# Optimization experiments

Measured on AMD Instinct MI355X. Metric: run time of the kernel, lower is better.

## Reference

```python
import jax, jax.numpy as jnp
import numpy as np

B, S, D = 2, 2048, 1024
H = 16
HD = D // H
MLP = 4096
EPS_LN = 1e-6
EPS_NORM = 1e-12
LOG_MAX = float(np.log(1.0 / 0.01))  # clamp cap for logit_scale


def setup_inputs() -> dict:
    key = jax.random.key(0)
    ks = jax.random.split(key, 12)
    sd = 0.02
    return {
        "x": jax.random.normal(ks[0], (B, S, D), jnp.float32),
        "wq": jax.random.normal(ks[1], (D, D), jnp.float32) * sd,
        "bq": jnp.zeros((D,), jnp.float32),
        "wk": jax.random.normal(ks[2], (D, D), jnp.float32) * sd,
        "bk": jnp.zeros((D,), jnp.float32),
        "wv": jax.random.normal(ks[3], (D, D), jnp.float32) * sd,
        "bv": jnp.zeros((D,), jnp.float32),
        "wo": jax.random.normal(ks[4], (D, D), jnp.float32) * sd,
        "bo": jnp.zeros((D,), jnp.float32),
        "w1": jax.random.normal(ks[5], (D, MLP), jnp.float32) * sd,
        "b1": jax.random.normal(ks[6], (MLP,), jnp.float32) * 1e-6,
        "w2": jax.random.normal(ks[7], (MLP, D), jnp.float32) * sd,
        "b2": jax.random.normal(ks[8], (D,), jnp.float32) * 1e-6,
        "ln1_g": jnp.ones((D,), jnp.float32),
        "ln1_b": jnp.zeros((D,), jnp.float32),
        "ln2_g": jnp.ones((D,), jnp.float32),
        "ln2_b": jnp.zeros((D,), jnp.float32),
        "logit_scale": jnp.log(10.0 * jnp.ones((H, 1, 1), jnp.float32)),
    }


def _layernorm(x, g, b):
    mu = jnp.mean(x, axis=-1, keepdims=True)
    var = jnp.var(x, axis=-1, keepdims=True)
    return (x - mu) * jax.lax.rsqrt(var + EPS_LN) * g + b


def _l2norm(x):
    n = jnp.linalg.norm(x, axis=-1, keepdims=True)
    return x / jnp.maximum(n, EPS_NORM)


def _split_heads(t):  # [B,S,D] -> [B,H,S,HD]
    return t.reshape(B, S, H, HD).transpose(0, 2, 1, 3)


def reference(x, wq, bq, wk, bk, wv, bv, wo, bo, w1, b1, w2, b2,
              ln1_g, ln1_b, ln2_g, ln2_b, logit_scale):
    h = x
    xn = _layernorm(x, ln1_g, ln1_b)
    q = _split_heads(xn @ wq + bq)
    k = _split_heads(xn @ wk + bk)
    v = _split_heads(xn @ wv + bv)
    # cosine attention: L2-normalize q,k, scale by clamped learnable exp temp
    scores = jnp.einsum("bhqd,bhkd->bhqk", _l2norm(q), _l2norm(k))
    scale = jnp.exp(jnp.minimum(logit_scale, LOG_MAX))  # [H,1,1]
    scores = scores * scale
    probs = jax.nn.softmax(scores, axis=-1)
    ctx = jnp.einsum("bhqk,bhkd->bhqd", probs, v)
    ctx = ctx.transpose(0, 2, 1, 3).reshape(B, S, D)
    x = ctx @ wo + bo + h
    h = x
    xn = _layernorm(x, ln2_g, ln2_b)
    y = jax.nn.gelu(xn @ w1 + b1, approximate=False) @ w2 + b2
    return y + h
```

## Files before the change

### kernel.cpp

```cpp
#include <hip/hip_runtime.h>
#include <hip/hip_bf16.h>
#include <math.h>

typedef unsigned short u16;
typedef unsigned int u32;
typedef __attribute__((ext_vector_type(8))) short bf16x8;
typedef __attribute__((ext_vector_type(4))) float f32x4;

#define S_LEN 2048
#define DM 1024
#define NH 16
#define HD 64
#define MLPD 4096
#define BSZ 2
#define NROWS (BSZ * S_LEN)
#define LOGMAX 4.60517018598809f

__device__ __forceinline__ u16 f2bf(float f) {
  u32 u = __float_as_uint(f);
  u32 r = (u + 0x7fffu + ((u >> 16) & 1u)) >> 16;
  return (u16)r;
}
__device__ __forceinline__ float bf2f(u16 h) { return __uint_as_float(((u32)h) << 16); }
__device__ __forceinline__ u32 pk2(float a, float b) {
  return (u32)f2bf(a) | ((u32)f2bf(b) << 16);
}
__device__ __forceinline__ void gld16(const void* g, void* l) {
  __builtin_amdgcn_global_load_lds(
      (const __attribute__((address_space(1))) void*)g,
      (__attribute__((address_space(3))) void*)l, 16, 0, 0);
}

__global__ __launch_bounds__(256) void ln_bf16(const float* __restrict__ x,
                                               const float* __restrict__ g,
                                               const float* __restrict__ b,
                                               u16* __restrict__ out) {
  const int row = blockIdx.x;
  const int t = threadIdx.x;
  const float* xr = x + (size_t)row * DM;
  float4 v = *reinterpret_cast<const float4*>(xr + t * 4);
  float s = v.x + v.y + v.z + v.w;
  float s2 = v.x * v.x + v.y * v.y + v.z * v.z + v.w * v.w;
#pragma unroll
  for (int off = 32; off > 0; off >>= 1) {
    s += __shfl_down(s, off);
    s2 += __shfl_down(s2, off);
  }
  __shared__ float red[8];
  __shared__ float mv[2];
  const int wid = t >> 6, lane = t & 63;
  if (lane == 0) { red[wid] = s; red[wid + 4] = s2; }
  __syncthreads();
  if (t == 0) {
    float ts = red[0] + red[1] + red[2] + red[3];
    float ts2 = red[4] + red[5] + red[6] + red[7];
    float mu = ts * (1.0f / DM);
    float var = ts2 * (1.0f / DM) - mu * mu;
    mv[0] = mu;
    mv[1] = rsqrtf(var + 1e-6f);
  }
  __syncthreads();
  const float mu = mv[0], rs = mv[1];
  float4 gv = *reinterpret_cast<const float4*>(g + t * 4);
  float4 bv = *reinterpret_cast<const float4*>(b + t * 4);
  float o0 = (v.x - mu) * rs * gv.x + bv.x;
  float o1 = (v.y - mu) * rs * gv.y + bv.y;
  float o2 = (v.z - mu) * rs * gv.z + bv.z;
  float o3 = (v.w - mu) * rs * gv.w + bv.w;
  uint2 o;
  o.x = pk2(o0, o1);
  o.y = pk2(o2, o3);
  *reinterpret_cast<uint2*>(out + (size_t)row * DM + t * 4) = o;
}

__global__ __launch_bounds__(256) void prep_weights(
    const float* __restrict__ wq, const float* __restrict__ wk, const float* __restrict__ wv,
    const float* __restrict__ wo, const float* __restrict__ w1, const float* __restrict__ w2,
    const float* __restrict__ bq, const float* __restrict__ bk, const float* __restrict__ bv,
    u16* __restrict__ wqkv_t, u16* __restrict__ wo_t, u16* __restrict__ w1_t,
    u16* __restrict__ w2_t, float* __restrict__ bqkv) {
  const int tid = threadIdx.x;
  int bid = blockIdx.x;
  if (bid < 12) {
    int i = bid * 256 + tid;
    bqkv[i] = i < 1024 ? bq[i] : (i < 2048 ? bk[i - 1024] : bv[i - 2048]);
  }
  const float* src;
  u16* dst;
  int K, N;
  if (bid < 768) {
    int m = bid >> 8;
    src = (m == 0) ? wq : (m == 1 ? wk : wv);
    dst = wqkv_t + (size_t)m * 1024 * 1024;
    K = 1024; N = 1024;
    bid &= 255;
  } else if (bid < 1024) {
    src = wo; dst = wo_t; K = 1024; N = 1024; bid -= 768;
  } else if (bid < 2048) {
    src = w1; dst = w1_t; K = 1024; N = 4096; bid -= 1024;
  } else {
    src = w2; dst = w2_t; K = 4096; N = 1024; bid -= 2048;
  }
  const int ktiles = K >> 6;
  const int k0 = (bid % ktiles) << 6, n0 = (bid / ktiles) << 6;
  __shared__ float tile[64][65];
#pragma unroll
  for (int p = 0; p < 4; ++p) {
    int r = p * 16 + (tid >> 4), c = (tid & 15) * 4;
    *reinterpret_cast<float4*>(&tile[r][c]) =
        *reinterpret_cast<const float4*>(&src[(size_t)(k0 + r) * N + n0 + c]);
  }
  __syncthreads();
#pragma unroll
  for (int p = 0; p < 4; ++p) {
    int n = p * 16 + (tid >> 4), k = (tid & 15) * 4;
    uint2 o;
    o.x = pk2(tile[k][n], tile[k + 1][n]);
    o.y = pk2(tile[k + 2][n], tile[k + 3][n]);
    *reinterpret_cast<uint2*>(&dst[(size_t)(n0 + n) * K + k0 + k]) = o;
  }
}

#define EPI_BIAS 0
#define EPI_GELU 1
#define EPI_RES 2

template <int EPI, int OUTBF>
__global__ __launch_bounds__(256) void gemm_bf16(
    const u16* __restrict__ A, const u16* __restrict__ Bt,
    const float* __restrict__ bias, const float* __restrict__ res,
    void* __restrict__ Cout, int M, int N, int K) {
  __shared__ u16 As[128 * 32];
  __shared__ u16 Bs[128 * 32];
  const int tid = threadIdx.x;
  const int wid = tid >> 6, lane = tid & 63;
  const int n0 = blockIdx.x * 128, m0 = blockIdx.y * 128;
  const int wr = wid >> 1, wc = wid & 1;

  f32x4 acc[4][4];
#pragma unroll
  for (int mi = 0; mi < 4; ++mi)
#pragma unroll
    for (int ni = 0; ni < 4; ++ni)
#pragma unroll
      for (int r = 0; r < 4; ++r) acc[mi][ni][r] = 0.0f;

  const int srow = lane >> 2;
  const int skc = (lane & 3) * 8;

  for (int k0 = 0; k0 < K; k0 += 32) {
#pragma unroll
    for (int i = 0; i < 2; ++i) {
      int c = wid * 2 + i;
      gld16(&A[(size_t)(m0 + c * 16 + srow) * K + k0 + skc], &As[c * 512]);
      gld16(&Bt[(size_t)(n0 + c * 16 + srow) * K + k0 + skc], &Bs[c * 512]);
    }
    __syncthreads();
    const int fr = lane & 15, fg = (lane >> 4) * 8;
    bf16x8 af[4], bfr[4];
#pragma unroll
    for (int mi = 0; mi < 4; ++mi)
      af[mi] = *reinterpret_cast<const bf16x8*>(&As[(wr * 64 + mi * 16 + fr) * 32 + fg]);
#pragma unroll
    for (int ni = 0; ni < 4; ++ni)
      bfr[ni] = *reinterpret_cast<const bf16x8*>(&Bs[(wc * 64 + ni * 16 + fr) * 32 + fg]);
#pragma unroll
    for (int mi = 0; mi < 4; ++mi)
#pragma unroll
      for (int ni = 0; ni < 4; ++ni)
        acc[mi][ni] =
            __builtin_amdgcn_mfma_f32_16x16x32_bf16(af[mi], bfr[ni], acc[mi][ni], 0, 0, 0);
    __syncthreads();
  }

  const int col0 = n0 + wc * 64 + (lane & 15);
  const int r4 = (lane >> 4) * 4;
#pragma unroll
  for (int ni = 0; ni < 4; ++ni) {
    const int col = col0 + ni * 16;
    const float bb = bias[col];
#pragma unroll
    for (int mi = 0; mi < 4; ++mi) {
      const int row = m0 + wr * 64 + mi * 16 + r4;
#pragma unroll
      for (int r = 0; r < 4; ++r) {
        float v = acc[mi][ni][r] + bb;
        if (EPI == EPI_GELU) v = 0.5f * v * (1.0f + erff(v * 0.70710678118654752f));
        if (EPI == EPI_RES) v += res[(size_t)(row + r) * N + col];
        if (OUTBF)
          ((u16*)Cout)[(size_t)(row + r) * N + col] = f2bf(v);
        else
          ((float*)Cout)[(size_t)(row + r) * N + col] = v;
      }
    }
  }
}

__global__ __launch_bounds__(256) void flash_mfma(const u16* __restrict__ qkv,
                                                  const float* __restrict__ lsc,
                                                  u16* __restrict__ ctx) {
  __shared__ u16 Ks[64 * 72];
  __shared__ u16 Vt[64 * 72];
  __shared__ u16 Ps[128 * 72];
  const int tid = threadIdx.x;
  const int wq = tid >> 6, lane = tid & 63;
  const int q0 = blockIdx.x * 128;
  const int bh = blockIdx.y, b = bh >> 4, h = bh & 15;
  const float scale = __expf(fminf(lsc[h], LOGMAX));
  const int fr = lane & 15, fgq = lane >> 4;

  bf16x8 qf[2][2];
#pragma unroll
  for (int qs = 0; qs < 2; ++qs) {
    float qv[2][8];
    float ssq = 0.0f;
#pragma unroll
    for (int ds = 0; ds < 2; ++ds) {
      const u16* src = qkv + (size_t)(b * S_LEN + q0 + wq * 32 + qs * 16 + fr) * 3072 +
                       h * 64 + ds * 32 + fgq * 8;
      uint4 u = *reinterpret_cast<const uint4*>(src);
      qv[ds][0] = bf2f(u.x & 0xffff); qv[ds][1] = bf2f(u.x >> 16);
      qv[ds][2] = bf2f(u.y & 0xffff); qv[ds][3] = bf2f(u.y >> 16);
      qv[ds][4] = bf2f(u.z & 0xffff); qv[ds][5] = bf2f(u.z >> 16);
      qv[ds][6] = bf2f(u.w & 0xffff); qv[ds][7] = bf2f(u.w >> 16);
#pragma unroll
      for (int j = 0; j < 8; ++j) ssq += qv[ds][j] * qv[ds][j];
    }
    ssq += __shfl_xor(ssq, 16);
    ssq += __shfl_xor(ssq, 32);
    float inv = 1.0f / fmaxf(sqrtf(ssq), 1e-12f);
#pragma unroll
    for (int ds = 0; ds < 2; ++ds)
#pragma unroll
      for (int j = 0; j < 8; ++j) qf[qs][ds][j] = (short)f2bf(qv[ds][j] * inv);
  }

  float den[2][4];
  f32x4 octx[2][4];
#pragma unroll
  for (int qs = 0; qs < 2; ++qs)
#pragma unroll
    for (int r = 0; r < 4; ++r) {
      den[qs][r] = 0.0f;
      octx[qs][r][0] = octx[qs][r][1] = octx[qs][r][2] = octx[qs][r][3] = 0.0f;
    }

  const int sr = tid >> 2, sseg = tid & 3;

  for (int kt = 0; kt < S_LEN / 64; ++kt) {
    {
      const u16* gk = qkv + (size_t)(b * S_LEN + kt * 64 + sr) * 3072 + 1024 + h * 64 + sseg * 8;
      uint4 u0 = *reinterpret_cast<const uint4*>(gk);
      uint4 u1 = *reinterpret_cast<const uint4*>(gk + 32);
      float kv[16];
      kv[0] = bf2f(u0.x & 0xffff); kv[1] = bf2f(u0.x >> 16);
      kv[2] = bf2f(u0.y & 0xffff); kv[3] = bf2f(u0.y >> 16);
      kv[4] = bf2f(u0.z & 0xffff); kv[5] = bf2f(u0.z >> 16);
      kv[6] = bf2f(u0.w & 0xffff); kv[7] = bf2f(u0.w >> 16);
      kv[8]  = bf2f(u1.x & 0xffff); kv[9]  = bf2f(u1.x >> 16);
      kv[10] = bf2f(u1.y & 0xffff); kv[11] = bf2f(u1.y >> 16);
      kv[12] = bf2f(u1.z & 0xffff); kv[13] = bf2f(u1.z >> 16);
      kv[14] = bf2f(u1.w & 0xffff); kv[15] = bf2f(u1.w >> 16);
      float ssk = 0.0f;
#pragma unroll
      for (int j = 0; j < 16; ++j) ssk += kv[j] * kv[j];
      ssk += __shfl_xor(ssk, 1);
      ssk += __shfl_xor(ssk, 2);
      float inv = 1.0f / fmaxf(sqrtf(ssk), 1e-12f);
      uint4 o;
      o.x = pk2(kv[0] * inv, kv[1] * inv);
      o.y = pk2(kv[2] * inv, kv[3] * inv);
      o.z = pk2(kv[4] * inv, kv[5] * inv);
      o.w = pk2(kv[6] * inv, kv[7] * inv);
      *reinterpret_cast<uint4*>(&Ks[sr * 72 + sseg * 8]) = o;
      o.x = pk2(kv[8] * inv, kv[9] * inv);
      o.y = pk2(kv[10] * inv, kv[11] * inv);
      o.z = pk2(kv[12] * inv, kv[13] * inv);
      o.w = pk2(kv[14] * inv, kv[15] * inv);
      *reinterpret_cast<uint4*>(&Ks[sr * 72 + 32 + sseg * 8]) = o;
      uint4 vv0 = *reinterpret_cast<const uint4*>(gk + 1024);
      uint4 vv1 = *reinterpret_cast<const uint4*>(gk + 1024 + 32);
      u16 ve[16] = {(u16)(vv0.x & 0xffff), (u16)(vv0.x >> 16), (u16)(vv0.y & 0xffff),
                    (u16)(vv0.y >> 16),    (u16)(vv0.z & 0xffff), (u16)(vv0.z >> 16),
                    (u16)(vv0.w & 0xffff), (u16)(vv0.w >> 16),
                    (u16)(vv1.x & 0xffff), (u16)(vv1.x >> 16), (u16)(vv1.y & 0xffff),
                    (u16)(vv1.y >> 16),    (u16)(vv1.z & 0xffff), (u16)(vv1.z >> 16),
                    (u16)(vv1.w & 0xffff), (u16)(vv1.w >> 16)};
#pragma unroll
      for (int j = 0; j < 8; ++j) {
        Vt[(sseg * 8 + j) * 72 + sr] = ve[j];
        Vt[(32 + sseg * 8 + j) * 72 + sr] = ve[8 + j];
      }
    }
    __syncthreads();

    f32x4 sc[2][4];
#pragma unroll
    for (int qs = 0; qs < 2; ++qs)
#pragma unroll
      for (int ks = 0; ks < 4; ++ks)
        sc[qs][ks][0] = sc[qs][ks][1] = sc[qs][ks][2] = sc[qs][ks][3] = 0.0f;
#pragma unroll
    for (int ks = 0; ks < 4; ++ks)
#pragma unroll
      for (int ds = 0; ds < 2; ++ds) {
        bf16x8 kf = *reinterpret_cast<const bf16x8*>(&Ks[(ks * 16 + fr) * 72 + ds * 32 + fgq * 8]);
#pragma unroll
        for (int qs = 0; qs < 2; ++qs)
          sc[qs][ks] = __builtin_amdgcn_mfma_f32_16x16x32_bf16(qf[qs][ds], kf, sc[qs][ks], 0, 0, 0);
      }

#pragma unroll
    for (int qs = 0; qs < 2; ++qs)
#pragma unroll
      for (int r = 0; r < 4; ++r) {
        const int prow = wq * 32 + qs * 16 + fgq * 4 + r;
        float ps = 0.0f;
#pragma unroll
        for (int ks = 0; ks < 4; ++ks) {
          float p = __expf(scale * (sc[qs][ks][r] - 1.0f));
          Ps[prow * 72 + ks * 16 + fr] = f2bf(p);
          ps += p;
        }
        ps += __shfl_xor(ps, 1);
        ps += __shfl_xor(ps, 2);
        ps += __shfl_xor(ps, 4);
        ps += __shfl_xor(ps, 8);
        den[qs][r] += ps;
      }

#pragma unroll
    for (int kvs = 0; kvs < 2; ++kvs) {
      bf16x8 pf0 = *reinterpret_cast<const bf16x8*>(&Ps[(wq * 32 + fr) * 72 + kvs * 32 + fgq * 8]);
      bf16x8 pf1 =
          *reinterpret_cast<const bf16x8*>(&Ps[(wq * 32 + 16 + fr) * 72 + kvs * 32 + fgq * 8]);
#pragma unroll
      for (int dsb = 0; dsb < 4; ++dsb) {
        bf16x8 vf = *reinterpret_cast<const bf16x8*>(&Vt[(dsb * 16 + fr) * 72 + kvs * 32 + fgq * 8]);
        octx[0][dsb] = __builtin_amdgcn_mfma_f32_16x16x32_bf16(pf0, vf, octx[0][dsb], 0, 0, 0);
        octx[1][dsb] = __builtin_amdgcn_mfma_f32_16x16x32_bf16(pf1, vf, octx[1][dsb], 0, 0, 0);
      }
    }
    __syncthreads();
  }

#pragma unroll
  for (int qs = 0; qs < 2; ++qs)
#pragma unroll
    for (int r = 0; r < 4; ++r) {
      float inv = 1.0f / den[qs][r];
      const int row = q0 + wq * 32 + qs * 16 + fgq * 4 + r;
#pragma unroll
      for (int dsb = 0; dsb < 4; ++dsb)
        ctx[(size_t)(b * S_LEN + row) * DM + h * 64 + dsb * 16 + fr] =
            f2bf(octx[qs][dsb][r] * inv);
    }
}

extern "C" void kernel_launch(void* const* d_in, const int* in_sizes, int n_in,
                              void* d_out, int out_size, void* d_ws, size_t ws_size,
                              hipStream_t stream) {
  const float* x    = (const float*)d_in[0];
  const float* wq   = (const float*)d_in[1];
  const float* bq   = (const float*)d_in[2];
  const float* wk   = (const float*)d_in[3];
  const float* bk   = (const float*)d_in[4];
  const float* wv   = (const float*)d_in[5];
  const float* bv   = (const float*)d_in[6];
  const float* wo   = (const float*)d_in[7];
  const float* bo   = (const float*)d_in[8];
  const float* w1   = (const float*)d_in[9];
  const float* b1   = (const float*)d_in[10];
  const float* w2   = (const float*)d_in[11];
  const float* b2   = (const float*)d_in[12];
  const float* ln1g = (const float*)d_in[13];
  const float* ln1b = (const float*)d_in[14];
  const float* ln2g = (const float*)d_in[15];
  const float* ln2b = (const float*)d_in[16];
  const float* lsc  = (const float*)d_in[17];

  char* ws = (char*)d_ws;
  u16* wqkv_t = (u16*)(ws + 0);
  u16* wo_t   = (u16*)(ws + 6291456);
  u16* w1_t   = (u16*)(ws + 8388608);
  u16* w2_t   = (u16*)(ws + 16777216);
  float* bqkv = (float*)(ws + 25165824);
  u16* xn     = (u16*)(ws + 25178112);
  u16* ctx    = (u16*)(ws + 33566720);
  float* x2   = (float*)(ws + 41955328);
  u16* qkv    = (u16*)(ws + 58732544);
  u16* h1     = qkv;

  prep_weights<<<dim3(3072), dim3(256), 0, stream>>>(wq, wk, wv, wo, w1, w2, bq, bk, bv,
                                                     wqkv_t, wo_t, w1_t, w2_t, bqkv);
  ln_bf16<<<dim3(NROWS), dim3(256), 0, stream>>>(x, ln1g, ln1b, xn);
  gemm_bf16<EPI_BIAS, 1><<<dim3(3072 / 128, NROWS / 128), dim3(256), 0, stream>>>(
      xn, wqkv_t, bqkv, nullptr, qkv, NROWS, 3072, 1024);
  flash_mfma<<<dim3(S_LEN / 128, BSZ * NH), dim3(256), 0, stream>>>(qkv, lsc, ctx);
  gemm_bf16<EPI_RES, 0><<<dim3(1024 / 128, NROWS / 128), dim3(256), 0, stream>>>(
      ctx, wo_t, bo, x, x2, NROWS, 1024, 1024);
  ln_bf16<<<dim3(NROWS), dim3(256), 0, stream>>>(x2, ln2g, ln2b, xn);
  gemm_bf16<EPI_GELU, 1><<<dim3(4096 / 128, NROWS / 128), dim3(256), 0, stream>>>(
      xn, w1_t, b1, nullptr, h1, NROWS, 4096, 1024);
  gemm_bf16<EPI_RES, 0><<<dim3(1024 / 128, NROWS / 128), dim3(256), 0, stream>>>(
      h1, w2_t, b2, x2, (float*)d_out, NROWS, 1024, 4096);
}
```

Measured before the change: 488.1 us.

## Fuse Q/K L2-normalization and V transpose into QKV GEMM epilogue

```diff
diff --git a/kernel.cpp b/kernel.cpp
--- a/kernel.cpp
+++ b/kernel.cpp
@@ -124,12 +124,14 @@
 #define EPI_BIAS 0
 #define EPI_GELU 1
 #define EPI_RES 2
+#define EPI_QKV 3
 
 template <int EPI, int OUTBF>
 __global__ __launch_bounds__(256) void gemm_bf16(
     const u16* __restrict__ A, const u16* __restrict__ Bt,
     const float* __restrict__ bias, const float* __restrict__ res,
-    void* __restrict__ Cout, int M, int N, int K) {
+    void* __restrict__ Cout, u16* __restrict__ qkx, u16* __restrict__ vtx,
+    int M, int N, int K) {
   __shared__ u16 As[128 * 32];
   __shared__ u16 Bs[128 * 32];
   const int tid = threadIdx.x;
@@ -175,10 +177,51 @@
 
   const int col0 = n0 + wc * 64 + (lane & 15);
   const int r4 = (lane >> 4) * 4;
+
+  if constexpr (EPI == EPI_QKV) {
+    float bias4[4];
+#pragma unroll
+    for (int ni = 0; ni < 4; ++ni) bias4[ni] = bias[col0 + ni * 16];
+    const bool isV = (n0 + wc * 64) >= 2048;
+#pragma unroll
+    for (int mi = 0; mi < 4; ++mi) {
+#pragma unroll
+      for (int r = 0; r < 4; ++r) {
+        const int row = m0 + wr * 64 + mi * 16 + r4 + r;
+        float v[4];
+#pragma unroll
+        for (int ni = 0; ni < 4; ++ni) v[ni] = acc[mi][ni][r] + bias4[ni];
+        if (!isV) {
+          float ss = v[0] * v[0] + v[1] * v[1] + v[2] * v[2] + v[3] * v[3];
+          ss += __shfl_xor(ss, 1);
+          ss += __shfl_xor(ss, 2);
+          ss += __shfl_xor(ss, 4);
+          ss += __shfl_xor(ss, 8);
+          float inv = 1.0f / fmaxf(sqrtf(ss), 1e-12f);
+#pragma unroll
+          for (int ni = 0; ni < 4; ++ni)
+            qkx[(size_t)row * 2048 + col0 + ni * 16] = f2bf(v[ni] * inv);
+        } else {
+          const int b = row >> 11, sl = row & 2047;
+#pragma unroll
+          for (int ni = 0; ni < 4; ++ni) {
+            const int col = col0 + ni * 16;
+            const int h = (col - 2048) >> 6, d = col & 63;
+            vtx[((size_t)(b * NH + h) * HD + d) * S_LEN + sl] = f2bf(v[ni]);
+          }
+        }
+      }
+    }
+    return;
+  }
+
+  float bias8[4];
+#pragma unroll
+  for (int ni = 0; ni < 4; ++ni) bias8[ni] = bias[col0 + ni * 16];
 #pragma unroll
   for (int ni = 0; ni < 4; ++ni) {
     const int col = col0 + ni * 16;
-    const float bb = bias[col];
+    const float bb = bias8[ni];
 #pragma unroll
     for (int mi = 0; mi < 4; ++mi) {
       const int row = m0 + wr * 64 + mi * 16 + r4;
@@ -196,7 +239,8 @@
   }
 }
 
-__global__ __launch_bounds__(256) void flash_mfma(const u16* __restrict__ qkv,
+__global__ __launch_bounds__(256) void flash_mfma(const u16* __restrict__ qk,
+                                                  const u16* __restrict__ vt,
                                                   const float* __restrict__ lsc,
                                                   u16* __restrict__ ctx) {
   __shared__ u16 Ks[64 * 72];
@@ -211,29 +255,12 @@
 
   bf16x8 qf[2][2];
 #pragma unroll
-  for (int qs = 0; qs < 2; ++qs) {
-    float qv[2][8];
-    float ssq = 0.0f;
-#pragma unroll
-    for (int ds = 0; ds < 2; ++ds) {
-      const u16* src = qkv + (size_t)(b * S_LEN + q0 + wq * 32 + qs * 16 + fr) * 3072 +
-                       h * 64 + ds * 32 + fgq * 8;
-      uint4 u = *reinterpret_cast<const uint4*>(src);
-      qv[ds][0] = bf2f(u.x & 0xffff); qv[ds][1] = bf2f(u.x >> 16);
-      qv[ds][2] = bf2f(u.y & 0xffff); qv[ds][3] = bf2f(u.y >> 16);
-      qv[ds][4] = bf2f(u.z & 0xffff); qv[ds][5] = bf2f(u.z >> 16);
-      qv[ds][6] = bf2f(u.w & 0xffff); qv[ds][7] = bf2f(u.w >> 16);
-#pragma unroll
-      for (int j = 0; j < 8; ++j) ssq += qv[ds][j] * qv[ds][j];
-    }
-    ssq += __shfl_xor(ssq, 16);
-    ssq += __shfl_xor(ssq, 32);
-    float inv = 1.0f / fmaxf(sqrtf(ssq), 1e-12f);
+  for (int qs = 0; qs < 2; ++qs)
 #pragma unroll
     for (int ds = 0; ds < 2; ++ds)
-#pragma unroll
-      for (int j = 0; j < 8; ++j) qf[qs][ds][j] = (short)f2bf(qv[ds][j] * inv);
-  }
+      qf[qs][ds] = *reinterpret_cast<const bf16x8*>(
+          &qk[(size_t)(b * S_LEN + q0 + wq * 32 + qs * 16 + fr) * 2048 + h * HD + ds * 32 +
+              fgq * 8]);
 
   float den[2][4];
   f32x4 octx[2][4];
@@ -249,48 +276,16 @@
 
   for (int kt = 0; kt < S_LEN / 64; ++kt) {
     {
-      const u16* gk = qkv + (size_t)(b * S_LEN + kt * 64 + sr) * 3072 + 1024 + h * 64 + sseg * 8;
-      uint4 u0 = *reinterpret_cast<const uint4*>(gk);
-      uint4 u1 = *reinterpret_cast<const uint4*>(gk + 32);
-      float kv[16];
-      kv[0] = bf2f(u0.x & 0xffff); kv[1] = bf2f(u0.x >> 16);
-      kv[2] = bf2f(u0.y & 0xffff); kv[3] = bf2f(u0.y >> 16);
-      kv[4] = bf2f(u0.z & 0xffff); kv[5] = bf2f(u0.z >> 16);
-      kv[6] = bf2f(u0.w & 0xffff); kv[7] = bf2f(u0.w >> 16);
-      kv[8]  = bf2f(u1.x & 0xffff); kv[9]  = bf2f(u1.x >> 16);
-      kv[10] = bf2f(u1.y & 0xffff); kv[11] = bf2f(u1.y >> 16);
-      kv[12] = bf2f(u1.z & 0xffff); kv[13] = bf2f(u1.z >> 16);
-      kv[14] = bf2f(u1.w & 0xffff); kv[15] = bf2f(u1.w >> 16);
-      float ssk = 0.0f;
-#pragma unroll
-      for (int j = 0; j < 16; ++j) ssk += kv[j] * kv[j];
-      ssk += __shfl_xor(ssk, 1);
-      ssk += __shfl_xor(ssk, 2);
-      float inv = 1.0f / fmaxf(sqrtf(ssk), 1e-12f);
-      uint4 o;
-      o.x = pk2(kv[0] * inv, kv[1] * inv);
-      o.y = pk2(kv[2] * inv, kv[3] * inv);
-      o.z = pk2(kv[4] * inv, kv[5] * inv);
-      o.w = pk2(kv[6] * inv, kv[7] * inv);
-      *reinterpret_cast<uint4*>(&Ks[sr * 72 + sseg * 8]) = o;
-      o.x = pk2(kv[8] * inv, kv[9] * inv);
-      o.y = pk2(kv[10] * inv, kv[11] * inv);
-      o.z = pk2(kv[12] * inv, kv[13] * inv);
-      o.w = pk2(kv[14] * inv, kv[15] * inv);
-      *reinterpret_cast<uint4*>(&Ks[sr * 72 + 32 + sseg * 8]) = o;
-      uint4 vv0 = *reinterpret_cast<const uint4*>(gk + 1024);
-      uint4 vv1 = *reinterpret_cast<const uint4*>(gk + 1024 + 32);
-      u16 ve[16] = {(u16)(vv0.x & 0xffff), (u16)(vv0.x >> 16), (u16)(vv0.y & 0xffff),
-                    (u16)(vv0.y >> 16),    (u16)(vv0.z & 0xffff), (u16)(vv0.z >> 16),
-                    (u16)(vv0.w & 0xffff), (u16)(vv0.w >> 16),
-                    (u16)(vv1.x & 0xffff), (u16)(vv1.x >> 16), (u16)(vv1.y & 0xffff),
-                    (u16)(vv1.y >> 16),    (u16)(vv1.z & 0xffff), (u16)(vv1.z >> 16),
-                    (u16)(vv1.w & 0xffff), (u16)(vv1.w >> 16)};
-#pragma unroll
-      for (int j = 0; j < 8; ++j) {
-        Vt[(sseg * 8 + j) * 72 + sr] = ve[j];
-        Vt[(32 + sseg * 8 + j) * 72 + sr] = ve[8 + j];
-      }
+      const u16* gkp = qk + (size_t)(b * S_LEN + kt * 64 + sr) * 2048 + 1024 + h * HD + sseg * 8;
+      *reinterpret_cast<uint4*>(&Ks[sr * 72 + sseg * 8]) =
+          *reinterpret_cast<const uint4*>(gkp);
+      *reinterpret_cast<uint4*>(&Ks[sr * 72 + 32 + sseg * 8]) =
+          *reinterpret_cast<const uint4*>(gkp + 32);
+      const u16* gvp = vt + (size_t)(bh * HD + sr) * S_LEN + kt * 64 + sseg * 8;
+      *reinterpret_cast<uint4*>(&Vt[sr * 72 + sseg * 8]) =
+          *reinterpret_cast<const uint4*>(gvp);
+      *reinterpret_cast<uint4*>(&Vt[sr * 72 + 32 + sseg * 8]) =
+          *reinterpret_cast<const uint4*>(gvp + 32);
     }
     __syncthreads();
 
@@ -352,7 +347,7 @@
       const int row = q0 + wq * 32 + qs * 16 + fgq * 4 + r;
 #pragma unroll
       for (int dsb = 0; dsb < 4; ++dsb)
-        ctx[(size_t)(b * S_LEN + row) * DM + h * 64 + dsb * 16 + fr] =
+        ctx[(size_t)(b * S_LEN + row) * DM + h * HD + dsb * 16 + fr] =
             f2bf(octx[qs][dsb][r] * inv);
     }
 }
@@ -386,22 +381,23 @@
   u16* w2_t   = (u16*)(ws + 16777216);
   float* bqkv = (float*)(ws + 25165824);
   u16* xn     = (u16*)(ws + 25178112);
-  u16* ctx    = (u16*)(ws + 33566720);
-  float* x2   = (float*)(ws + 41955328);
-  u16* qkv    = (u16*)(ws + 58732544);
-  u16* h1     = qkv;
+  float* x2   = (float*)(ws + 33566720);
+  u16* qkbuf  = (u16*)(ws + 50343936);
+  u16* vtbuf  = (u16*)(ws + 67121152);
+  u16* ctx    = (u16*)(ws + 75509760);
+  u16* h1     = qkbuf;
 
   prep_weights<<<dim3(3072), dim3(256), 0, stream>>>(wq, wk, wv, wo, w1, w2, bq, bk, bv,
                                                      wqkv_t, wo_t, w1_t, w2_t, bqkv);
   ln_bf16<<<dim3(NROWS), dim3(256), 0, stream>>>(x, ln1g, ln1b, xn);
-  gemm_bf16<EPI_BIAS, 1><<<dim3(3072 / 128, NROWS / 128), dim3(256), 0, stream>>>(
-      xn, wqkv_t, bqkv, nullptr, qkv, NROWS, 3072, 1024);
-  flash_mfma<<<dim3(S_LEN / 128, BSZ * NH), dim3(256), 0, stream>>>(qkv, lsc, ctx);
+  gemm_bf16<EPI_QKV, 1><<<dim3(3072 / 128, NROWS / 128), dim3(256), 0, stream>>>(
+      xn, wqkv_t, bqkv, nullptr, nullptr, qkbuf, vtbuf, NROWS, 3072, 1024);
+  flash_mfma<<<dim3(S_LEN / 128, BSZ * NH), dim3(256), 0, stream>>>(qkbuf, vtbuf, lsc, ctx);
   gemm_bf16<EPI_RES, 0><<<dim3(1024 / 128, NROWS / 128), dim3(256), 0, stream>>>(
-      ctx, wo_t, bo, x, x2, NROWS, 1024, 1024);
+      ctx, wo_t, bo, x, x2, nullptr, nullptr, NROWS, 1024, 1024);
   ln_bf16<<<dim3(NROWS), dim3(256), 0, stream>>>(x2, ln2g, ln2b, xn);
   gemm_bf16<EPI_GELU, 1><<<dim3(4096 / 128, NROWS / 128), dim3(256), 0, stream>>>(
-      xn, w1_t, b1, nullptr, h1, NROWS, 4096, 1024);
+      xn, w1_t, b1, nullptr, h1, nullptr, nullptr, NROWS, 4096, 1024);
   gemm_bf16<EPI_RES, 0><<<dim3(1024 / 128, NROWS / 128), dim3(256), 0, stream>>>(
-      h1, w2_t, b2, x2, (float*)d_out, NROWS, 1024, 4096);
-}
+      h1, w2_t, b2, x2, (float*)d_out, nullptr, nullptr, NROWS, 1024, 4096);
+}
```

After: 481.3 us. No clear change (-1.4%).
